# Kernel optimization log

Hardware: AMD Instinct MI355X
Metric: run time of the kernel (lower is better)

The kernel has to match this reference:

```python
import jax, jax.numpy as jnp
import numpy as np

D_MODEL = 768
N_HEADS = 12
D_FF = 3072
EPS = 1e-6


def _xavier(key, shape):
    fan_out, fan_in = shape
    a = jnp.sqrt(6.0 / (fan_in + fan_out))
    return jax.random.uniform(key, shape, jnp.float32, -a, a)


def setup_inputs() -> dict:
    key = jax.random.key(0)
    ks = jax.random.split(key, 10)
    B, S = 2, 2048
    x = jax.random.normal(ks[0], (B, S, D_MODEL), jnp.float32)
    mask = jax.random.randint(ks[1], (B, 1, 1, S), 0, 2) == 1
    wq = _xavier(ks[2], (D_MODEL, D_MODEL)); bq = jnp.zeros((D_MODEL,))
    wk = _xavier(ks[3], (D_MODEL, D_MODEL)); bk = jnp.zeros((D_MODEL,))
    wv = _xavier(ks[4], (D_MODEL, D_MODEL)); bv = jnp.zeros((D_MODEL,))
    wo = _xavier(ks[5], (D_MODEL, D_MODEL)); bo = jnp.zeros((D_MODEL,))
    w1 = _xavier(ks[6], (D_FF, D_MODEL)); b1 = jnp.zeros((D_FF,))
    w2 = _xavier(ks[7], (D_MODEL, D_FF)); b2 = jnp.zeros((D_MODEL,))
    g1 = jnp.ones((D_MODEL,)); be1 = jnp.zeros((D_MODEL,))
    g2 = jnp.ones((D_MODEL,)); be2 = jnp.zeros((D_MODEL,))
    return dict(x=x, mask=mask, wq=wq, bq=bq, wk=wk, bk=bk, wv=wv, bv=bv,
                wo=wo, bo=bo, w1=w1, b1=b1, w2=w2, b2=b2,
                g1=g1, be1=be1, g2=g2, be2=be2)


def _layer_norm(x, gamma, beta):
    # torch: mean + unbiased std (ddof=1), divide by (std + eps)
    mean = jnp.mean(x, axis=-1, keepdims=True)
    std = jnp.std(x, axis=-1, keepdims=True, ddof=1)
    return gamma * (x - mean) / (std + EPS) + beta


def _encoder(x, mask, wq, bq, wk, bk, wv, bv, wo, bo, w1, b1, w2, b2, g1, be1, g2, be2):
    B, S, D = x.shape
    H, Dk = N_HEADS, D // N_HEADS
    q = (x @ wq.T + bq).reshape(B, S, H, Dk).transpose(0, 2, 1, 3)
    k = (x @ wk.T + bk).reshape(B, S, H, Dk).transpose(0, 2, 1, 3)
    v = (x @ wv.T + bv).reshape(B, S, H, Dk).transpose(0, 2, 1, 3)
    scores = jnp.einsum('bhqd,bhkd->bhqk', q, k) / jnp.sqrt(jnp.float32(Dk))
    scores = jnp.where(mask, jnp.float32(-1e9), scores)
    probs = jax.nn.softmax(scores, axis=-1)
    attn = jnp.einsum('bhqk,bhkd->bhqd', probs, v)
    attn = attn.transpose(0, 2, 1, 3).reshape(B, S, D)
    attn = attn @ wo.T + bo
    x = _layer_norm(x + attn, g1, be1)
    ff = jax.nn.relu(x @ w1.T + b1) @ w2.T + b2
    return _layer_norm(x + ff, g2, be2)


def reference(x, mask, wq, bq, wk, bk, wv, bv, wo, bo, w1, b1, w2, b2, g1, be1, g2, be2):
    return _encoder(x, mask, wq, bq, wk, bk, wv, bv, wo, bo, w1, b1, w2, b2, g1, be1, g2, be2)
```

## Files before the change

### kernel.cpp

```cpp
#include <hip/hip_runtime.h>
#include <hip/hip_bf16.h>

typedef __hip_bfloat16 bf16;
typedef unsigned short ushort;
typedef __attribute__((ext_vector_type(8))) short short8;
typedef __attribute__((ext_vector_type(4))) float f32x4;

__device__ __forceinline__ float b2f(bf16 h) { return __bfloat162float(h); }
__device__ __forceinline__ bf16 f2b(float f) { return __float2bfloat16(f); }
__device__ __forceinline__ ushort f2bu(float f) {
    bf16 t = __float2bfloat16(f);
    ushort u;
    __builtin_memcpy(&u, &t, 2);
    return u;
}
__device__ __forceinline__ float bits2f(unsigned int u16) {
    unsigned int v = u16 << 16;
    float f;
    __builtin_memcpy(&f, &v, 4);
    return f;
}

__device__ __forceinline__ void gload16(const void* g, void* l) {
    __builtin_amdgcn_global_load_lds(
        (const __attribute__((address_space(1))) void*)g,
        (__attribute__((address_space(3))) void*)l, 16, 0, 0);
}

__global__ void detect_dtype_kernel(const unsigned short* __restrict__ x,
                                    int* __restrict__ flag) {
    __shared__ int cnt;
    if (threadIdx.x == 0) cnt = 0;
    __syncthreads();
    int local = 0;
    for (int i = threadIdx.x; i < 2048; i += 256) {
        float v = bits2f((unsigned int)x[i]);
        if (!(fabsf(v) < 1e4f)) local++;
    }
    atomicAdd(&cnt, local);
    __syncthreads();
    if (threadIdx.x == 0) flag[0] = (cnt >= 8) ? 1 : 0;
}

__device__ __forceinline__ void load8f_rt(const void* p, int isf, float* f) {
    if (isf) {
        const float* q = (const float*)p;
        float4 a = *(const float4*)q;
        float4 b = *(const float4*)(q + 4);
        f[0] = a.x; f[1] = a.y; f[2] = a.z; f[3] = a.w;
        f[4] = b.x; f[5] = b.y; f[6] = b.z; f[7] = b.w;
    } else {
        uint4 u = *(const uint4*)p;
        f[0] = bits2f(u.x & 0xffffu); f[1] = bits2f(u.x >> 16);
        f[2] = bits2f(u.y & 0xffffu); f[3] = bits2f(u.y >> 16);
        f[4] = bits2f(u.z & 0xffffu); f[5] = bits2f(u.z >> 16);
        f[6] = bits2f(u.w & 0xffffu); f[7] = bits2f(u.w >> 16);
    }
}
__device__ __forceinline__ float loadf_rt(const void* p, int isf, size_t i) {
    return isf ? ((const float*)p)[i] : bits2f(((const ushort*)p)[i]);
}

__global__ __launch_bounds__(256) void conv_all_k(
    const int* __restrict__ dflag,
    const void* __restrict__ x,
    const void* __restrict__ wq, const void* __restrict__ wk,
    const void* __restrict__ wv, const void* __restrict__ wo,
    const void* __restrict__ w1, const void* __restrict__ w2,
    const void* __restrict__ bq, const void* __restrict__ bk,
    const void* __restrict__ bv, const void* __restrict__ bo,
    const void* __restrict__ b1, const void* __restrict__ b2,
    const void* __restrict__ g1, const void* __restrict__ be1,
    const void* __restrict__ g2, const void* __restrict__ be2,
    ushort* __restrict__ xb, ushort* __restrict__ wall,
    float* __restrict__ vall)
{
    const int isf = dflag[0];
    const int esz = isf ? 4 : 2;
    const int gt = blockIdx.x * 256 + threadIdx.x;
    const int stride = gridDim.x * 256;

    for (int v = gt; v < 393216; v += stride) {
        float f[8];
        load8f_rt((const char*)x + (size_t)v * 8 * esz, isf, f);
        unsigned int wd[4];
        #pragma unroll
        for (int i = 0; i < 4; ++i)
            wd[i] = (unsigned int)f2bu(f[2 * i]) | ((unsigned int)f2bu(f[2 * i + 1]) << 16);
        *(uint4*)(xb + (size_t)v * 8) = make_uint4(wd[0], wd[1], wd[2], wd[3]);
    }
    for (int v = gt; v < 884736; v += stride) {
        const void* src; int loc;
        if (v < 73728)        { src = wq; loc = v; }
        else if (v < 147456)  { src = wk; loc = v - 73728; }
        else if (v < 221184)  { src = wv; loc = v - 147456; }
        else if (v < 294912)  { src = wo; loc = v - 221184; }
        else if (v < 589824)  { src = w1; loc = v - 294912; }
        else                  { src = w2; loc = v - 589824; }
        float f[8];
        load8f_rt((const char*)src + (size_t)loc * 8 * esz, isf, f);
        unsigned int wd[4];
        #pragma unroll
        for (int i = 0; i < 4; ++i)
            wd[i] = (unsigned int)f2bu(f[2 * i]) | ((unsigned int)f2bu(f[2 * i + 1]) << 16);
        *(uint4*)(wall + (size_t)v * 8) = make_uint4(wd[0], wd[1], wd[2], wd[3]);
    }
    for (int i = gt; i < 9984; i += stride) {
        const void* s; int l;
        if (i < 768)       { s = bq;  l = i; }
        else if (i < 1536) { s = bk;  l = i - 768; }
        else if (i < 2304) { s = bv;  l = i - 1536; }
        else if (i < 3072) { s = bo;  l = i - 2304; }
        else if (i < 6144) { s = b1;  l = i - 3072; }
        else if (i < 6912) { s = b2;  l = i - 6144; }
        else if (i < 7680) { s = g1;  l = i - 6912; }
        else if (i < 8448) { s = be1; l = i - 7680; }
        else if (i < 9216) { s = g2;  l = i - 8448; }
        else               { s = be2; l = i - 9216; }
        vall[i] = loadf_rt(s, isf, l);
    }
}

template <int BM>
__device__ __forceinline__ void gemm_bf16_body(
    const ushort* __restrict__ A, const ushort* __restrict__ Bw,
    const float* __restrict__ bias, ushort* __restrict__ Cb,
    float* __restrict__ Cf, int N, int K, int bm, int bn, int relu)
{
    __shared__ __align__(16) ushort As[2][BM][64];
    __shared__ __align__(16) ushort Bs[2][128][64];
    const int tid = threadIdx.x;
    const int w = tid >> 6, lane = tid & 63;
    const int quad = lane >> 4, l15 = lane & 15;
    constexpr int FM = BM / 32;
    const int wr = (w >> 1) * (BM / 2), wc = (w & 1) * 64;

    constexpr int CA = (BM * 128) / 4096;
    constexpr int CB = 4;
    size_t aoff[CA]; int albase[CA];
    #pragma unroll
    for (int c = 0; c < CA; ++c) {
        int byte = c * 4096 + tid * 16;
        int row = byte >> 7, colb = byte & 127;
        int csrc = colb ^ ((row & 7) << 4);
        aoff[c] = (size_t)(bm + row) * K + (csrc >> 1);
        albase[c] = c * 4096 + w * 1024;
    }
    size_t boff[CB]; int blbase[CB];
    #pragma unroll
    for (int c = 0; c < CB; ++c) {
        int byte = c * 4096 + tid * 16;
        int row = byte >> 7, colb = byte & 127;
        int csrc = colb ^ ((row & 7) << 4);
        boff[c] = (size_t)(bn + row) * K + (csrc >> 1);
        blbase[c] = c * 4096 + w * 1024;
    }

    f32x4 acc[FM][4];
    #pragma unroll
    for (int i = 0; i < FM; ++i)
        #pragma unroll
        for (int j = 0; j < 4; ++j) acc[i][j] = (f32x4){0.f, 0.f, 0.f, 0.f};

    constexpr int ASZ = BM * 128;
    constexpr int BSZ = 128 * 128;

#define STAGE(buf, k0)                                                        \
    {                                                                         \
        char* ab = (char*)As + (buf) * ASZ;                                   \
        char* bb = (char*)Bs + (buf) * BSZ;                                   \
        _Pragma("unroll")                                                     \
        for (int c = 0; c < CA; ++c)                                          \
            gload16(A + aoff[c] + (k0), ab + albase[c]);                      \
        _Pragma("unroll")                                                     \
        for (int c = 0; c < CB; ++c)                                          \
            gload16(Bw + boff[c] + (k0), bb + blbase[c]);                     \
    }

    const int NT = K >> 6;
    STAGE(0, 0);
    int cur = 0;
    for (int t = 0; t < NT; ++t) {
        __syncthreads();
        if (t + 1 < NT) STAGE(cur ^ 1, (t + 1) * 64);

        const ushort (*Asb)[64] = As[cur];
        const ushort (*Bsb)[64] = Bs[cur];
        short8 af[FM][2], bfr[4][2];
        #pragma unroll
        for (int i = 0; i < FM; ++i) {
            int r = wr + i * 16 + l15;
            int sw = (r & 7) << 3;
            af[i][0] = *(const short8*)&Asb[r][(quad * 8) ^ sw];
            af[i][1] = *(const short8*)&Asb[r][(32 + quad * 8) ^ sw];
        }
        #pragma unroll
        for (int j = 0; j < 4; ++j) {
            int r = wc + j * 16 + l15;
            int sw = (r & 7) << 3;
            bfr[j][0] = *(const short8*)&Bsb[r][(quad * 8) ^ sw];
            bfr[j][1] = *(const short8*)&Bsb[r][(32 + quad * 8) ^ sw];
        }
        #pragma unroll
        for (int h = 0; h < 2; ++h)
            #pragma unroll
            for (int i = 0; i < FM; ++i)
                #pragma unroll
                for (int j = 0; j < 4; ++j)
                    acc[i][j] = __builtin_amdgcn_mfma_f32_16x16x32_bf16(
                        af[i][h], bfr[j][h], acc[i][j], 0, 0, 0);
        cur ^= 1;
    }
#undef STAGE

    #pragma unroll
    for (int j = 0; j < 4; ++j) {
        int col = bn + wc + j * 16 + l15;
        float bv = bias[col];
        #pragma unroll
        for (int i = 0; i < FM; ++i) {
            int row0 = bm + wr + i * 16 + quad * 4;
            #pragma unroll
            for (int r = 0; r < 4; ++r) {
                float vv = acc[i][j][r] + bv;
                if (relu) vv = fmaxf(vv, 0.f);
                size_t idx = (size_t)(row0 + r) * N + col;
                if (Cb) Cb[idx] = f2bu(vv);
                if (Cf) Cf[idx] = vv;
            }
        }
    }
}

__device__ __forceinline__ int xcd_swz(int bid, int nwg) {
    int cpx = nwg >> 3;
    return (bid & 7) * cpx + (bid >> 3);
}

template <int BM>
__global__ __launch_bounds__(256) void gemm_b(
    const ushort* __restrict__ A, const ushort* __restrict__ Bw,
    const float* __restrict__ bias, ushort* __restrict__ Cb,
    float* __restrict__ Cf, int N, int K, int relu)
{
    int nwg = gridDim.x * gridDim.y;
    int bid = xcd_swz(blockIdx.y * gridDim.x + blockIdx.x, nwg);
    int bx = bid % gridDim.x, by = bid / gridDim.x;
    gemm_bf16_body<BM>(A, Bw, bias, Cb, Cf, N, K, by * BM, bx * 128, relu);
}

__global__ __launch_bounds__(256) void gemm_qkv_b(
    const ushort* __restrict__ x, const ushort* __restrict__ wall,
    const float* __restrict__ vall,
    ushort* __restrict__ qb, ushort* __restrict__ kb, ushort* __restrict__ vb)
{
    int bid = xcd_swz(blockIdx.y * 18 + blockIdx.x, 576);
    int bx = bid % 18, by = bid / 18;
    const int mat = bx / 6;
    const int bn = (bx % 6) * 128;
    const ushort* W = wall + (size_t)mat * 589824;
    const float* Bi = vall + mat * 768;
    ushort* O = (mat == 0) ? qb : (mat == 1) ? kb : vb;
    gemm_bf16_body<128>(x, W, Bi, O, nullptr, 768, 768, by * 128, bn, 0);
}

__global__ __launch_bounds__(512) void attn_mfma_b(
    const ushort* __restrict__ q, const ushort* __restrict__ k,
    const ushort* __restrict__ v, const int* __restrict__ mask,
    float* __restrict__ opart, float* __restrict__ mlbuf)
{
    const int S = 2048, D = 768;
    const size_t NXD = 3145728;
    const float SC2 = 0.125f * 1.44269504088896f;
    __shared__ __align__(16) ushort Ks[64][72];
    __shared__ __align__(16) ushort Vt[64][72];
    __shared__ __align__(16) ushort Ps[8][16][72];
    __shared__ float mkAll[1024];

    const int tid = threadIdx.x;
    const int w = tid >> 6, lane = tid & 63;
    const int quad = lane >> 4, l15 = lane & 15;

    const int bx = xcd_swz(blockIdx.x, 768);
    const int part = bx / 384;
    const int rest = bx - part * 384;
    const int q0 = (rest & 15) * 128;
    const int h = (rest >> 4) % 12;
    const int b = rest / 192;
    const int kbase = part * 1024;

    #pragma unroll
    for (int i = 0; i < 2; ++i) {
        int idx = tid + i * 512;
        mkAll[idx] = mask[b * S + kbase + idx] ? -30000.f : 0.f;
    }

    const size_t qrow = (size_t)(b * S + q0 + w * 16 + l15) * D + h * 64;
    const short8 aQ0 = *(const short8*)&q[qrow + quad * 8];
    const short8 aQ1 = *(const short8*)&q[qrow + 32 + quad * 8];

    short8 ones;
    #pragma unroll
    for (int j = 0; j < 8; ++j) ones[j] = (short)0x3F80;

    f32x4 o[4], lacc;
    #pragma unroll
    for (int i = 0; i < 4; ++i) o[i] = (f32x4){0.f, 0.f, 0.f, 0.f};
    lacc = (f32x4){0.f, 0.f, 0.f, 0.f};
    float m_run = -3.0e38f;

    const int sr = tid >> 3;
    const int sc0 = (tid & 7) * 8;

    const ushort* kp = k + (size_t)(b * S + kbase + sr) * D + h * 64 + sc0;
    const ushort* vp = v + (size_t)(b * S + kbase + lane) * D + h * 64 + w * 8;
    uint4 ka = *(const uint4*)kp;
    uint4 va = *(const uint4*)vp;

    for (int kt = 0; kt < 16; ++kt) {
        __syncthreads();
        *(uint4*)&Ks[sr][sc0] = ka;
        {
            alignas(16) ushort tmp[8];
            *(uint4*)tmp = va;
            #pragma unroll
            for (int i = 0; i < 8; ++i) Vt[w * 8 + i][lane] = tmp[i];
        }
        __syncthreads();

        if (kt + 1 < 16) {
            kp += 64 * D;
            vp += 64 * D;
            ka = *(const uint4*)kp;
            va = *(const uint4*)vp;
        }

        const float* mk = &mkAll[kt * 64];
        float scv[4][4];
        float vm = -3.0e38f;
        __builtin_amdgcn_s_setprio(1);
        #pragma unroll
        for (int s = 0; s < 4; ++s) {
            short8 bk0 = *(const short8*)&Ks[s * 16 + l15][quad * 8];
            short8 bk1 = *(const short8*)&Ks[s * 16 + l15][32 + quad * 8];
            f32x4 c = (f32x4){0.f, 0.f, 0.f, 0.f};
            c = __builtin_amdgcn_mfma_f32_16x16x32_bf16(aQ0, bk0, c, 0, 0, 0);
            c = __builtin_amdgcn_mfma_f32_16x16x32_bf16(aQ1, bk1, c, 0, 0, 0);
            float mb = mk[s * 16 + l15];
            #pragma unroll
            for (int r = 0; r < 4; ++r) {
                float val = __builtin_fmaf(c[r], SC2, mb);
                scv[s][r] = val;
                vm = fmaxf(vm, val);
            }
        }
        __builtin_amdgcn_s_setprio(0);
        vm = fmaxf(vm, __shfl_xor(vm, 1, 16));
        vm = fmaxf(vm, __shfl_xor(vm, 2, 16));
        vm = fmaxf(vm, __shfl_xor(vm, 4, 16));
        vm = fmaxf(vm, __shfl_xor(vm, 8, 16));

        if (__any(vm > m_run + 11.0f)) {
            float mn = fmaxf(m_run, vm);
            float alpha = exp2f(m_run - mn);
            #pragma unroll
            for (int s = 0; s < 4; ++s) o[s] *= alpha;
            lacc *= alpha;
            m_run = mn;
        }

        #pragma unroll
        for (int r = 0; r < 4; ++r)
            #pragma unroll
            for (int s = 0; s < 4; ++s)
                Ps[w][quad * 4 + r][(s * 16 + l15) ^ (quad << 4)] =
                    f2bu(exp2f(scv[s][r] - m_run));
        asm volatile("s_waitcnt lgkmcnt(0)" ::: "memory");

        {
            const int pswz = (l15 >> 2) << 4;
            short8 aP0 = *(const short8*)&Ps[w][l15][(quad * 8) ^ pswz];
            short8 aP1 = *(const short8*)&Ps[w][l15][(32 + quad * 8) ^ pswz];
            __builtin_amdgcn_s_setprio(1);
            lacc = __builtin_amdgcn_mfma_f32_16x16x32_bf16(aP0, ones, lacc, 0, 0, 0);
            lacc = __builtin_amdgcn_mfma_f32_16x16x32_bf16(aP1, ones, lacc, 0, 0, 0);
            #pragma unroll
            for (int s = 0; s < 4; ++s) {
                short8 bv0 = *(const short8*)&Vt[s * 16 + l15][quad * 8];
                short8 bv1 = *(const short8*)&Vt[s * 16 + l15][32 + quad * 8];
                o[s] = __builtin_amdgcn_mfma_f32_16x16x32_bf16(aP0, bv0, o[s], 0, 0, 0);
                o[s] = __builtin_amdgcn_mfma_f32_16x16x32_bf16(aP1, bv1, o[s], 0, 0, 0);
            }
            __builtin_amdgcn_s_setprio(0);
        }
    }

    const size_t obase = (size_t)part * NXD +
                         (size_t)(b * S + q0 + w * 16) * D + h * 64;
    #pragma unroll
    for (int r = 0; r < 4; ++r)
        #pragma unroll
        for (int s = 0; s < 4; ++s)
            opart[obase + (size_t)(quad * 4 + r) * D + s * 16 + l15] = o[s][r];
    if (l15 == 0) {
        #pragma unroll
        for (int r = 0; r < 4; ++r) {
            int row = b * S + q0 + w * 16 + quad * 4 + r;
            size_t mi = (((size_t)part * 4096 + row) * 12 + h) * 2;
            mlbuf[mi] = m_run;
            mlbuf[mi + 1] = lacc[r];
        }
    }
}

__global__ __launch_bounds__(256) void attn_combine(
    const float* __restrict__ opart, const float* __restrict__ mlbuf,
    ushort* __restrict__ ctx)
{
    const size_t NXD = 3145728;
    const int row = blockIdx.x;
    const int tid = threadIdx.x;
    #pragma unroll
    for (int i = 0; i < 3; ++i) {
        int d = tid + i * 256;
        int h = d >> 6;
        size_t m0i = ((size_t)row * 12 + h) * 2;
        size_t m1i = (((size_t)4096 + row) * 12 + h) * 2;
        float m0 = mlbuf[m0i], l0 = mlbuf[m0i + 1];
        float m1 = mlbuf[m1i], l1 = mlbuf[m1i + 1];
        float m = fmaxf(m0, m1);
        float e0 = exp2f(m0 - m), e1 = exp2f(m1 - m);
        float inv = 1.f / (l0 * e0 + l1 * e1);
        size_t idx = (size_t)row * 768 + d;
        float val = (opart[idx] * e0 + opart[NXD + idx] * e1) * inv;
        ctx[idx] = f2bu(val);
    }
}

__global__ __launch_bounds__(256) void ln1_kernel(
    const int* __restrict__ dflag,
    const void* __restrict__ xa, const float* __restrict__ r,
    const float* __restrict__ gamma, const float* __restrict__ beta,
    ushort* __restrict__ outb, float* __restrict__ outf)
{
    const int isf = dflag[0];
    const int row = blockIdx.x;
    const int tid = threadIdx.x;
    __shared__ float red[4];
    const size_t base = (size_t)row * 768;

    float x[3];
    #pragma unroll
    for (int i = 0; i < 3; ++i) {
        int d = tid + i * 256;
        x[i] = loadf_rt(xa, isf, base + d) + r[base + d];
    }

    float s = x[0] + x[1] + x[2];
    #pragma unroll
    for (int off = 32; off > 0; off >>= 1) s += __shfl_down(s, off, 64);
    if ((tid & 63) == 0) red[tid >> 6] = s;
    __syncthreads();
    float mean = (red[0] + red[1] + red[2] + red[3]) * (1.f / 768.f);
    __syncthreads();

    float vsum = 0.f;
    #pragma unroll
    for (int i = 0; i < 3; ++i) {
        float dd = x[i] - mean;
        vsum += dd * dd;
    }
    #pragma unroll
    for (int off = 32; off > 0; off >>= 1) vsum += __shfl_down(vsum, off, 64);
    if ((tid & 63) == 0) red[tid >> 6] = vsum;
    __syncthreads();
    float var = (red[0] + red[1] + red[2] + red[3]) * (1.f / 767.f);
    float inv = 1.f / (sqrtf(var) + 1e-6f);

    #pragma unroll
    for (int i = 0; i < 3; ++i) {
        int d = tid + i * 256;
        float y = gamma[d] * (x[i] - mean) * inv + beta[d];
        outb[base + d] = f2bu(y);
        outf[base + d] = y;
    }
}

__global__ __launch_bounds__(256) void ln2_kernel(
    const int* __restrict__ dflag,
    const float* __restrict__ a, const float* __restrict__ r,
    const float* __restrict__ gamma, const float* __restrict__ beta,
    void* __restrict__ out)
{
    const int isf = dflag[0];
    const int row = blockIdx.x;
    const int tid = threadIdx.x;
    __shared__ float red[4];
    const size_t base = (size_t)row * 768;

    float x[3];
    #pragma unroll
    for (int i = 0; i < 3; ++i) {
        int d = tid + i * 256;
        x[i] = a[base + d] + r[base + d];
    }

    float s = x[0] + x[1] + x[2];
    #pragma unroll
    for (int off = 32; off > 0; off >>= 1) s += __shfl_down(s, off, 64);
    if ((tid & 63) == 0) red[tid >> 6] = s;
    __syncthreads();
    float mean = (red[0] + red[1] + red[2] + red[3]) * (1.f / 768.f);
    __syncthreads();

    float vsum = 0.f;
    #pragma unroll
    for (int i = 0; i < 3; ++i) {
        float dd = x[i] - mean;
        vsum += dd * dd;
    }
    #pragma unroll
    for (int off = 32; off > 0; off >>= 1) vsum += __shfl_down(vsum, off, 64);
    if ((tid & 63) == 0) red[tid >> 6] = vsum;
    __syncthreads();
    float var = (red[0] + red[1] + red[2] + red[3]) * (1.f / 767.f);
    float inv = 1.f / (sqrtf(var) + 1e-6f);

    #pragma unroll
    for (int i = 0; i < 3; ++i) {
        int d = tid + i * 256;
        float y = gamma[d] * (x[i] - mean) * inv + beta[d];
        if (isf) ((float*)out)[base + d] = y;
        else     ((ushort*)out)[base + d] = f2bu(y);
    }
}

extern "C" void kernel_launch(void* const* d_in, const int* in_sizes, int n_in,
                              void* d_out, int out_size, void* d_ws, size_t ws_size,
                              hipStream_t stream) {
    const size_t nxd = 3145728;
    char* base = (char*)d_ws;
    int* dflag = (int*)base;

    char* p = base + 256;
    ushort* xb   = (ushort*)p; p += nxd * 2;
    ushort* wall = (ushort*)p; p += 7077888ull * 2;
    float*  vall = (float*)p;  p += 40960;
    ushort* qb   = (ushort*)p;
    ushort* kb   = qb + nxd;
    ushort* vb   = kb + nxd;
    ushort* ctx  = vb + nxd;
    ushort* ff1b = qb;
    p += 4 * nxd * 2;
    float* oproj = (float*)p;
    float* ff2f  = oproj;
    p += nxd * 4;
    ushort* ln1b = (ushort*)p; p += nxd * 2;
    float*  ln1f = (float*)p;  p += nxd * 4;

    float* opart = oproj;
    float* mlbuf = oproj + 2 * nxd;

    const int* mask = (const int*)d_in[1];
    dim3 blk(256);

    detect_dtype_kernel<<<dim3(1), blk, 0, stream>>>(
        (const unsigned short*)d_in[0], dflag);

    conv_all_k<<<dim3(1024), blk, 0, stream>>>(dflag,
        d_in[0], d_in[2], d_in[4], d_in[6], d_in[8], d_in[10], d_in[12],
        d_in[3], d_in[5], d_in[7], d_in[9], d_in[11], d_in[13],
        d_in[14], d_in[15], d_in[16], d_in[17], xb, wall, vall);

    gemm_qkv_b<<<dim3(18, 32), blk, 0, stream>>>(xb, wall, vall, qb, kb, vb);

    attn_mfma_b<<<dim3(768), dim3(512), 0, stream>>>(qb, kb, vb, mask, opart, mlbuf);
    attn_combine<<<dim3(4096), blk, 0, stream>>>(opart, mlbuf, ctx);

    gemm_b<64><<<dim3(6, 64), blk, 0, stream>>>(
        ctx, wall + 1769472, vall + 2304, nullptr, oproj, 768, 768, 0);

    ln1_kernel<<<dim3(4096), blk, 0, stream>>>(dflag,
        d_in[0], oproj, vall + 6912, vall + 7680, ln1b, ln1f);

    gemm_b<128><<<dim3(24, 32), blk, 0, stream>>>(
        ln1b, wall + 2359296, vall + 3072, ff1b, nullptr, 3072, 768, 1);

    gemm_b<64><<<dim3(6, 64), blk, 0, stream>>>(
        ff1b, wall + 4718592, vall + 6144, nullptr, ff2f, 768, 3072, 0);

    ln2_kernel<<<dim3(4096), blk, 0, stream>>>(dflag,
        ln1f, ff2f, vall + 8448, vall + 9216, d_out);
}
```

Baseline: 324.1 us.

## Split-K the output-projection and FFN2 GEMMs, fusing partial sums into layernorm

The two GEMMs with N=768 (attention output projection and the second FFN matmul) now run as a two-way split-K launch that writes two fp32 partial outputs, and the bias is applied only in the first split. The following layernorm kernels sum both partials along with the residual. The aim is to double the workgroup count for these narrow GEMMs so the GPU is better filled. The cost is an extra fp32 partial buffer to write and read, and workspace buffers are reassigned to hold it.

```diff
diff --git a/kernel.cpp b/kernel.cpp
--- a/kernel.cpp
+++ b/kernel.cpp
@@ -125,7 +125,8 @@
 __device__ __forceinline__ void gemm_bf16_body(
     const ushort* __restrict__ A, const ushort* __restrict__ Bw,
     const float* __restrict__ bias, ushort* __restrict__ Cb,
-    float* __restrict__ Cf, int N, int K, int bm, int bn, int relu)
+    float* __restrict__ Cf, int N, int K, int kstart, int klen,
+    int bm, int bn, int relu)
 {
     __shared__ __align__(16) ushort As[2][BM][64];
     __shared__ __align__(16) ushort Bs[2][128][64];
@@ -177,12 +178,12 @@
             gload16(Bw + boff[c] + (k0), bb + blbase[c]);                     \
     }
 
-    const int NT = K >> 6;
-    STAGE(0, 0);
+    const int NT = klen >> 6;
+    STAGE(0, kstart);
     int cur = 0;
     for (int t = 0; t < NT; ++t) {
         __syncthreads();
-        if (t + 1 < NT) STAGE(cur ^ 1, (t + 1) * 64);
+        if (t + 1 < NT) STAGE(cur ^ 1, kstart + (t + 1) * 64);
 
         const ushort (*Asb)[64] = As[cur];
         const ushort (*Bsb)[64] = Bs[cur];
@@ -216,7 +217,7 @@
     #pragma unroll
     for (int j = 0; j < 4; ++j) {
         int col = bn + wc + j * 16 + l15;
-        float bv = bias[col];
+        float bv = bias ? bias[col] : 0.f;
         #pragma unroll
         for (int i = 0; i < FM; ++i) {
             int row0 = bm + wr + i * 16 + quad * 4;
@@ -246,7 +247,22 @@
     int nwg = gridDim.x * gridDim.y;
     int bid = xcd_swz(blockIdx.y * gridDim.x + blockIdx.x, nwg);
     int bx = bid % gridDim.x, by = bid / gridDim.x;
-    gemm_bf16_body<BM>(A, Bw, bias, Cb, Cf, N, K, by * BM, bx * 128, relu);
+    gemm_bf16_body<BM>(A, Bw, bias, Cb, Cf, N, K, 0, K, by * BM, bx * 128, relu);
+}
+
+template <int BM>
+__global__ __launch_bounds__(256) void gemm_ksplit(
+    const ushort* __restrict__ A, const ushort* __restrict__ Bw,
+    const float* __restrict__ bias, float* __restrict__ Cf, int N, int K)
+{
+    const int part = blockIdx.z;
+    int nwg = gridDim.x * gridDim.y;
+    int bid = xcd_swz(blockIdx.y * gridDim.x + blockIdx.x, nwg);
+    int bx = bid % gridDim.x, by = bid / gridDim.x;
+    const int kh = K >> 1;
+    gemm_bf16_body<BM>(A, Bw, part ? nullptr : bias, nullptr,
+                       Cf + (size_t)part * 3145728, N, K,
+                       part * kh, kh, by * BM, bx * 128, 0);
 }
 
 __global__ __launch_bounds__(256) void gemm_qkv_b(
@@ -261,7 +277,7 @@
     const ushort* W = wall + (size_t)mat * 589824;
     const float* Bi = vall + mat * 768;
     ushort* O = (mat == 0) ? qb : (mat == 1) ? kb : vb;
-    gemm_bf16_body<128>(x, W, Bi, O, nullptr, 768, 768, by * 128, bn, 0);
+    gemm_bf16_body<128>(x, W, Bi, O, nullptr, 768, 768, 0, 768, by * 128, bn, 0);
 }
 
 __global__ __launch_bounds__(512) void attn_mfma_b(
@@ -439,7 +455,8 @@
 
 __global__ __launch_bounds__(256) void ln1_kernel(
     const int* __restrict__ dflag,
-    const void* __restrict__ xa, const float* __restrict__ r,
+    const void* __restrict__ xa, const float* __restrict__ r0,
+    const float* __restrict__ r1,
     const float* __restrict__ gamma, const float* __restrict__ beta,
     ushort* __restrict__ outb, float* __restrict__ outf)
 {
@@ -453,7 +470,7 @@
     #pragma unroll
     for (int i = 0; i < 3; ++i) {
         int d = tid + i * 256;
-        x[i] = loadf_rt(xa, isf, base + d) + r[base + d];
+        x[i] = loadf_rt(xa, isf, base + d) + r0[base + d] + r1[base + d];
     }
 
     float s = x[0] + x[1] + x[2];
@@ -488,7 +505,8 @@
 
 __global__ __launch_bounds__(256) void ln2_kernel(
     const int* __restrict__ dflag,
-    const float* __restrict__ a, const float* __restrict__ r,
+    const float* __restrict__ a, const float* __restrict__ f0,
+    const float* __restrict__ f1,
     const float* __restrict__ gamma, const float* __restrict__ beta,
     void* __restrict__ out)
 {
@@ -502,7 +520,7 @@
     #pragma unroll
     for (int i = 0; i < 3; ++i) {
         int d = tid + i * 256;
-        x[i] = a[base + d] + r[base + d];
+        x[i] = a[base + d] + f0[base + d] + f1[base + d];
     }
 
     float s = x[0] + x[1] + x[2];
@@ -552,14 +570,14 @@
     ushort* ctx  = vb + nxd;
     ushort* ff1b = qb;
     p += 4 * nxd * 2;
-    float* oproj = (float*)p;
-    float* ff2f  = oproj;
-    p += nxd * 4;
-    ushort* ln1b = (ushort*)p; p += nxd * 2;
-    float*  ln1f = (float*)p;  p += nxd * 4;
-
-    float* opart = oproj;
-    float* mlbuf = oproj + 2 * nxd;
+    float* dbuf = (float*)p; p += nxd * 4;
+    float* ebuf = (float*)p; p += nxd * 4;
+    float* gbuf = (float*)p; p += nxd * 4;
+
+    float* opart = dbuf;
+    float* mlbuf = gbuf;
+    ushort* ln1b = xb;
+    float* ln1f = gbuf;
 
     const int* mask = (const int*)d_in[1];
     dim3 blk(256);
@@ -577,18 +595,18 @@
     attn_mfma_b<<<dim3(768), dim3(512), 0, stream>>>(qb, kb, vb, mask, opart, mlbuf);
     attn_combine<<<dim3(4096), blk, 0, stream>>>(opart, mlbuf, ctx);
 
-    gemm_b<64><<<dim3(6, 64), blk, 0, stream>>>(
-        ctx, wall + 1769472, vall + 2304, nullptr, oproj, 768, 768, 0);
+    gemm_ksplit<64><<<dim3(6, 64, 2), blk, 0, stream>>>(
+        ctx, wall + 1769472, vall + 2304, dbuf, 768, 768);
 
     ln1_kernel<<<dim3(4096), blk, 0, stream>>>(dflag,
-        d_in[0], oproj, vall + 6912, vall + 7680, ln1b, ln1f);
+        d_in[0], dbuf, ebuf, vall + 6912, vall + 7680, ln1b, ln1f);
 
     gemm_b<128><<<dim3(24, 32), blk, 0, stream>>>(
         ln1b, wall + 2359296, vall + 3072, ff1b, nullptr, 3072, 768, 1);
 
-    gemm_b<64><<<dim3(6, 64), blk, 0, stream>>>(
-        ff1b, wall + 4718592, vall + 6144, nullptr, ff2f, 768, 3072, 0);
+    gemm_ksplit<64><<<dim3(6, 64, 2), blk, 0, stream>>>(
+        ff1b, wall + 4718592, vall + 6144, dbuf, 768, 3072);
 
     ln2_kernel<<<dim3(4096), blk, 0, stream>>>(dflag,
-        ln1f, ff2f, vall + 8448, vall + 9216, d_out);
-}
+        ln1f, dbuf, ebuf, vall + 8448, vall + 9216, d_out);
+}
```

After: 318.4 us. Within noise of the previous version (-1.8%).
